# Kernel tuning notes

Hardware: AMD Instinct MI355X
Metric: run time of the kernel (lower is better)

## Reference

```python
import jax, jax.numpy as jnp
import numpy as np

DILATIONS = (1, 2, 4, 8, 16, 32, 64, 128)  # new_dilation doubles across all blocks*layers
BN_EPS = 1e-5


def conv1x1(x, w, b):
    # x: [B,C,N,T], w: [O,C], b: [O]
    return jnp.einsum('oc,bcnt->bont', w, x) + b[None, :, None, None]


def dilated_conv(x, w, b, d):
    T = x.shape[-1]
    y = jnp.einsum('oc,bcnt->bont', w[:, :, 0], x[..., :T - d]) \
      + jnp.einsum('oc,bcnt->bont', w[:, :, 1], x[..., d:])
    return y + b[None, :, None, None]


def graph_conv(x, supports, w, b):
    # gcn module, order=2, diag_mode='self_and_neighbor' (A unchanged), use_power=False
    outs = [x]
    for A in supports:
        h = x
        for _ in range(2):  # order
            h = jnp.einsum('bcvt,vw->bcwt', h, A)  # nconv: 'ncvl,vw->ncwl'
            outs.append(h)
    return conv1x1(jnp.concatenate(outs, axis=1), w, b)


def setup_inputs() -> dict:
    key = jax.random.key(0)
    B, Cin, N, T = 8, 2, 500, 256
    rc, dc, sc, ec, od, L, R = 32, 32, 256, 512, 12, 8, 10
    ks = jax.random.split(key, 24)
    s = 0.1
    return {
        'x': jax.random.normal(ks[0], (B, Cin, N, T), jnp.float32),
        'A0': jax.random.uniform(ks[1], (N, N), jnp.float32),
        'start_w': jax.random.normal(ks[2], (rc, Cin), jnp.float32) * s,
        'start_b': jnp.zeros((rc,), jnp.float32),
        'filt_w': jax.random.normal(ks[3], (L, dc, rc, 2), jnp.float32) * s,
        'filt_b': jnp.zeros((L, dc), jnp.float32),
        'gate_w': jax.random.normal(ks[4], (L, dc, rc, 2), jnp.float32) * s,
        'gate_b': jnp.zeros((L, dc), jnp.float32),
        'skip_w': jax.random.normal(ks[5], (L, sc, dc), jnp.float32) * s,
        'skip_b': jnp.zeros((L, sc), jnp.float32),
        'gcn_w': jax.random.normal(ks[6], (L, rc, 5 * dc), jnp.float32) * s,  # (order*supports+1)*c_in = 160
        'gcn_b': jnp.zeros((L, rc), jnp.float32),
        'bn_g': jnp.ones((L, rc), jnp.float32),
        'bn_b': jnp.zeros((L, rc), jnp.float32),
        'nodevec1': jax.random.normal(ks[7], (N, R), jnp.float32),
        'nodevec2': jax.random.normal(ks[8], (R, N), jnp.float32),
        'end1_w': jax.random.normal(ks[9], (ec, sc), jnp.float32) * s,
        'end1_b': jnp.zeros((ec,), jnp.float32),
        'end2_w': jax.random.normal(ks[10], (od, ec), jnp.float32) * s,
        'end2_b': jnp.zeros((od,), jnp.float32),
    }


def reference(x, A0, start_w, start_b, filt_w, filt_b, gate_w, gate_b,
              skip_w, skip_b, gcn_w, gcn_b, bn_g, bn_b,
              nodevec1, nodevec2, end1_w, end1_b, end2_w, end2_b):
    # adaptive adjacency: softmax(relu(E1 @ E2), dim=1)
    adp = jax.nn.softmax(jax.nn.relu(nodevec1 @ nodevec2), axis=1)
    supports = [A0, adp]

    h = conv1x1(x, start_w, start_b)  # [B,32,N,T]
    skip = None
    for i, d in enumerate(DILATIONS):
        residual = h
        f = jnp.tanh(dilated_conv(residual, filt_w[i], filt_b[i], d))
        g = jax.nn.sigmoid(dilated_conv(residual, gate_w[i], gate_b[i], d))
        h = f * g
        s = conv1x1(h, skip_w[i], skip_b[i])
        skip = s if skip is None else s + skip[..., -s.shape[-1]:]
        h = graph_conv(h, supports, gcn_w[i], gcn_b[i])
        h = h + residual[..., -h.shape[-1]:]
        # BatchNorm2d in eval mode: running_mean=0, running_var=1
        h = h / jnp.sqrt(1.0 + BN_EPS) * bn_g[i][None, :, None, None] + bn_b[i][None, :, None, None]

    out = jax.nn.relu(skip)
    out = jax.nn.relu(conv1x1(out, end1_w, end1_b))
    out = conv1x1(out, end2_w, end2_b)  # [B,12,N,1]
    return out
```

## Files before the change

kernel.cpp:

```cpp
#include <hip/hip_runtime.h>
#include <cstdint>
#include <cstddef>

#define NN 500
#define KP 512

typedef _Float16 f16;
typedef _Float16 half8 __attribute__((ext_vector_type(8)));
typedef float floatx4 __attribute__((ext_vector_type(4)));

struct PassSet {
  const f16* A[10];
  const f16* B[10];
};

__global__ __launch_bounds__(256) void adp_kernel(const float* __restrict__ e1,
                                                  const float* __restrict__ e2,
                                                  float* __restrict__ adp) {
  int r = blockIdx.x;
  int tid = threadIdx.x;
  __shared__ float red[256];
  __shared__ float e1row[16];
  if (tid < 10) e1row[tid] = e1[r * 10 + tid];
  __syncthreads();
  float z0, z1 = 0.f;
  {
    float acc = 0.f;
#pragma unroll
    for (int k = 0; k < 10; k++) acc += e1row[k] * e2[k * NN + tid];
    z0 = fmaxf(acc, 0.f);
  }
  bool has1 = (tid + 256) < NN;
  if (has1) {
    float acc = 0.f;
#pragma unroll
    for (int k = 0; k < 10; k++) acc += e1row[k] * e2[k * NN + tid + 256];
    z1 = fmaxf(acc, 0.f);
  }
  float mx = has1 ? fmaxf(z0, z1) : z0;
  red[tid] = mx;
  __syncthreads();
  for (int s = 128; s > 0; s >>= 1) {
    if (tid < s) red[tid] = fmaxf(red[tid], red[tid + s]);
    __syncthreads();
  }
  mx = red[0];
  __syncthreads();
  float ex0 = __expf(z0 - mx);
  float ex1 = has1 ? __expf(z1 - mx) : 0.f;
  red[tid] = ex0 + ex1;
  __syncthreads();
  for (int s = 128; s > 0; s >>= 1) {
    if (tid < s) red[tid] += red[tid + s];
    __syncthreads();
  }
  float inv = 1.f / red[0];
  adp[r * NN + tid] = ex0 * inv;
  if (has1) adp[r * NN + tid + 256] = ex1 * inv;
}

__global__ __launch_bounds__(256) void xt_kernel(const float* __restrict__ x,
                                                 float* __restrict__ xT) {
  __shared__ float tile[32][33];
  int tx = threadIdx.x & 31, ty = threadIdx.x >> 5;
  int n0 = blockIdx.x * 32, t0 = blockIdx.y * 32, bc = blockIdx.z;
#pragma unroll
  for (int rr = 0; rr < 4; rr++) {
    int n = n0 + ty + rr * 8, t = t0 + tx;
    tile[ty + rr * 8][tx] = (n < NN) ? x[((size_t)bc * NN + n) * 256 + t] : 0.f;
  }
  __syncthreads();
#pragma unroll
  for (int rr = 0; rr < 4; rr++) {
    int t = t0 + ty + rr * 8, n = n0 + tx;
    if (n < NN) xT[((size_t)bc * 256 + t) * NN + n] = tile[tx][ty + rr * 8];
  }
}

__global__ __launch_bounds__(256) void wtr_kernel(const float* __restrict__ fw,
                                                  const float* __restrict__ gw,
                                                  float* __restrict__ fwT,
                                                  float* __restrict__ gwT) {
  int idx = blockIdx.x * 256 + threadIdx.x;
  if (idx >= 16384) return;
  int c = idx & 31;
  int rest = idx >> 5;
  int tap = rest & 1;
  int cpi = rest >> 1;
  int cp = cpi & 31, i = cpi >> 5;
  size_t src = (((size_t)(i * 32 + c) * 32 + cp) * 2) + tap;
  fwT[idx] = fw[src];
  gwT[idx] = gw[src];
}

__global__ __launch_bounds__(256) void bt_kernel(const float* __restrict__ src,
                                                 f16* __restrict__ hi,
                                                 f16* __restrict__ lo) {
  int idx = blockIdx.x * 256 + threadIdx.x;
  int w = idx >> 9, v = idx & 511;
  float x = (w < NN && v < NN) ? src[v * NN + w] : 0.f;
  f16 h = (f16)x;
  hi[idx] = h;
  lo[idx] = (f16)(x - (float)h);
}

__global__ __launch_bounds__(512) void sq_kernel(const float* __restrict__ srcA,
                                                 const float* __restrict__ srcB,
                                                 f16* __restrict__ hiA, f16* __restrict__ loA,
                                                 f16* __restrict__ hiB, f16* __restrict__ loB) {
  const float* src = blockIdx.y == 0 ? srcA : srcB;
  f16* hi = blockIdx.y == 0 ? hiA : hiB;
  f16* lo = blockIdx.y == 0 ? loA : loB;
  int v = blockIdx.x;
  int w = threadIdx.x;
  __shared__ float vrow[512];
  vrow[w] = (v < NN && w < NN) ? src[v * NN + w] : 0.f;
  __syncthreads();
  float acc = 0.f;
  if (v < NN && w < NN) {
#pragma unroll 4
    for (int u = 0; u < NN; u++) acc = fmaf(vrow[u], src[u * NN + w], acc);
  }
  size_t o = (size_t)w * 512 + v;
  f16 h = (f16)acc;
  hi[o] = h;
  lo[o] = (f16)(acc - (float)h);
}

__global__ __launch_bounds__(256) void padzero_kernel(uint32_t* __restrict__ slab, int R) {
  int idx = blockIdx.x * 256 + threadIdx.x;
  int total = 6 * R * 6;
  if (idx >= total) return;
  int a = idx / (R * 6);
  int rem = idx - a * R * 6;
  int row = rem / 6;
  int q = rem - row * 6;
  slab[(size_t)a * R * 256 + (size_t)row * 256 + 250 + q] = 0u;
}

template <bool FUSED>
__global__ __launch_bounds__(256, 4) void dcm_kernel(
    const float* __restrict__ hprev, const float* __restrict__ xT,
    const float* __restrict__ sw, const float* __restrict__ sb,
    const float* __restrict__ fw, const float* __restrict__ fb,
    const float* __restrict__ gw, const float* __restrict__ gb,
    const float* __restrict__ cw, const float* __restrict__ cb,
    float* __restrict__ Hout,
    f16* __restrict__ P1a,
    f16* __restrict__ P2aH, f16* __restrict__ P2aL,
    f16* __restrict__ P1b,
    f16* __restrict__ P2bH, f16* __restrict__ P2bL,
    float* __restrict__ tapL,
    int Lp, int L, int b0) {
  int j = blockIdx.x, bb = blockIdx.y;
  int n0 = blockIdx.z * 256 + threadIdx.x;
  bool ok = (n0 < NN);
  int nc = ok ? n0 : (NN - 1);
  size_t base = ((size_t)(bb * 32) * Lp + 2 * j) * NN;
  size_t cs = (size_t)Lp * NN;
  float x00 = 0.f, x01 = 0.f, x10 = 0.f, x11 = 0.f;
  if (FUSED) {
    const float* xb = xT + (size_t)(b0 + bb) * 2 * 256 * NN;
    x00 = xb[(size_t)(2 * j) * NN + nc];
    x01 = xb[(size_t)(2 * j + 1) * NN + nc];
    x10 = xb[(size_t)(256 + 2 * j) * NN + nc];
    x11 = xb[(size_t)(256 + 2 * j + 1) * NN + nc];
  }
  float accf[32], accg[32];
#pragma unroll
  for (int c = 0; c < 32; c++) {
    accf[c] = fb[c];
    accg[c] = gb[c];
  }
#pragma unroll 2
  for (int cp = 0; cp < 32; cp++) {
    float v0, v1;
    if (FUSED) {
      float w0 = sw[cp * 2], w1 = sw[cp * 2 + 1], bc = sb[cp];
      v0 = fmaf(w0, x00, fmaf(w1, x10, bc));
      v1 = fmaf(w0, x01, fmaf(w1, x11, bc));
    } else {
      const float* hp = hprev + base + cp * cs;
      v0 = hp[nc];
      v1 = hp[NN + nc];
    }
    const float* fwp = fw + cp * 64;
    const float* gwp = gw + cp * 64;
#pragma unroll
    for (int c = 0; c < 32; c++) {
      float fw0 = fwp[c], fw1 = fwp[32 + c];
      float gw0 = gwp[c], gw1 = gwp[32 + c];
      accf[c] = fmaf(fw0, v0, accf[c]);
      accf[c] = fmaf(fw1, v1, accf[c]);
      accg[c] = fmaf(gw0, v0, accg[c]);
      accg[c] = fmaf(gw1, v1, accg[c]);
    }
  }
  float FG[32];
#pragma unroll
  for (int c = 0; c < 32; c++) {
    float E0 = __expf(2.f * accf[c]);
    float th0 = 1.f - 2.f / (E0 + 1.f);
    float sg0 = 1.f / (1.f + __expf(-accg[c]));
    FG[c] = th0 * sg0;
  }
  if (j == L - 1 && ok) {
    size_t tbase = ((size_t)(b0 + bb) * 32) * NN;
#pragma unroll
    for (int c = 0; c < 32; c++) {
      tapL[tbase + (size_t)c * NN + n0] = FG[c];
    }
  }
  if (Hout == nullptr) return;
#pragma unroll 2
  for (int c = 0; c < 32; c++) {
    const float* wr = cw + c * 160;
    float cbc = cb[c];
    float h0 = cbc, p10 = 0.f, p20 = 0.f, q10 = 0.f, q20 = 0.f;
#pragma unroll
    for (int cp = 0; cp < 32; cp++) {
      float w0 = wr[cp], w1 = wr[32 + cp], w2 = wr[64 + cp];
      float w3 = wr[96 + cp], w4 = wr[128 + cp];
      float f0 = FG[cp];
      h0  = fmaf(w0, f0, h0);
      p10 = fmaf(w1, f0, p10);
      p20 = fmaf(w2, f0, p20);
      q10 = fmaf(w3, f0, q10);
      q20 = fmaf(w4, f0, q20);
    }
    if (FUSED) {
      float sw0 = sw[c * 2], sw1 = sw[c * 2 + 1], sbc = sb[c];
      h0 += fmaf(sw0, x01, fmaf(sw1, x11, sbc));
    } else {
      const float* hr = hprev + ((size_t)(bb * 32 + c) * Lp + 2 * j + 1) * NN;
      h0 += hr[nc];
    }
    if (ok) {
      size_t mi = (size_t)(bb * 32 + c) * L + j;
      size_t o = mi * KP;
      f16 t;
      Hout[mi * NN + n0] = h0;
      P1a[o + n0] = (f16)p10;
      t = (f16)p20; P2aH[o + n0] = t; P2aL[o + n0] = (f16)(p20 - (float)t);
      P1b[o + n0] = (f16)q10;
      t = (f16)q20; P2bH[o + n0] = t; P2bL[o + n0] = (f16)(q20 - (float)t);
    }
  }
}

__global__ __launch_bounds__(256) void mfma_gcn(PassSet s,
    const float* __restrict__ Cin, float* __restrict__ Out, int M,
    const float* __restrict__ bng, const float* __restrict__ bnb, int lshift) {
  __shared__ f16 As[128 * 32];
  __shared__ f16 Bs[128 * 32];
  int tid = threadIdx.x;
  int wave = tid >> 6, lane = tid & 63;
  int wm = wave >> 1, wn = wave & 1;
  int m0 = blockIdx.x * 128;
  int n0 = blockIdx.y * 128;
  int lm = lane & 15, kq = lane >> 4;
  int srow = tid >> 2, sc = tid & 3;
  int ar0 = m0 + srow;      if (ar0 > M - 1) ar0 = M - 1;
  int ar1 = m0 + srow + 64; if (ar1 > M - 1) ar1 = M - 1;
  size_t ag0 = (size_t)ar0 * KP + sc * 8;
  size_t ag1 = (size_t)ar1 * KP + sc * 8;
  size_t bg0 = (size_t)(n0 + srow) * KP + sc * 8;
  size_t bg1 = (size_t)(n0 + srow + 64) * KP + sc * 8;
  int sl0 = srow * 32 + ((sc ^ ((srow >> 1) & 3)) << 3);
  int sl1 = sl0 + 64 * 32;
  int ach = kq ^ ((lm >> 1) & 3);

  floatx4 acc[4][4];
#pragma unroll
  for (int i = 0; i < 4; i++)
#pragma unroll
    for (int j = 0; j < 4; j++) acc[i][j] = (floatx4){0.f, 0.f, 0.f, 0.f};

  float4 pa0, pa1, pb0, pb1;
  {
    const f16* Ap = s.A[0];
    const f16* Bp = s.B[0];
    pa0 = *(const float4*)(Ap + ag0);
    pa1 = *(const float4*)(Ap + ag1);
    pb0 = *(const float4*)(Bp + bg0);
    pb1 = *(const float4*)(Bp + bg1);
  }
#pragma unroll
  for (int p = 0; p < 10; p++) {
    const f16* __restrict__ Ap = s.A[p];
    const f16* __restrict__ Bp = s.B[p];
    const f16* __restrict__ Apn = s.A[p < 9 ? p + 1 : p];
    const f16* __restrict__ Bpn = s.B[p < 9 ? p + 1 : p];
    for (int k0 = 0; k0 < KP; k0 += 32) {
      __syncthreads();
      *(float4*)(As + sl0) = pa0;
      *(float4*)(As + sl1) = pa1;
      *(float4*)(Bs + sl0) = pb0;
      *(float4*)(Bs + sl1) = pb1;
      __syncthreads();
      {
        bool lastk = (k0 == KP - 32);
        const f16* An = lastk ? Apn : Ap;
        const f16* Bn = lastk ? Bpn : Bp;
        int kn = lastk ? 0 : k0 + 32;
        pa0 = *(const float4*)(An + ag0 + kn);
        pa1 = *(const float4*)(An + ag1 + kn);
        pb0 = *(const float4*)(Bn + bg0 + kn);
        pb1 = *(const float4*)(Bn + bg1 + kn);
      }
      half8 a[4];
#pragma unroll
      for (int i = 0; i < 4; i++)
        a[i] = *(const half8*)(As + (wm * 64 + i * 16 + lm) * 32 + ach * 8);
#pragma unroll
      for (int j = 0; j < 4; j++) {
        half8 b = *(const half8*)(Bs + (wn * 64 + j * 16 + lm) * 32 + ach * 8);
#pragma unroll
        for (int i = 0; i < 4; i++)
          acc[i][j] = __builtin_amdgcn_mfma_f32_16x16x32_f16(a[i], b, acc[i][j], 0, 0, 0);
      }
    }
  }
  int cn = lane & 15, rq = lane >> 4;
  float rs = rsqrtf(1.f + 1e-5f);
#pragma unroll
  for (int i = 0; i < 4; i++) {
#pragma unroll
    for (int r = 0; r < 4; r++) {
      int row = m0 + wm * 64 + i * 16 + rq * 4 + r;
      if (row < M) {
        int c = (row >> lshift) & 31;
        float scale = bng[c] * rs;
        float bias = bnb[c];
#pragma unroll
        for (int j = 0; j < 4; j++) {
          int col = n0 + wn * 64 + j * 16 + cn;
          if (col < NN) {
            size_t o = (size_t)row * NN + col;
            Out[o] = (acc[i][j][r] + Cin[o]) * scale + bias;
          }
        }
      }
    }
  }
}

#define NB 20
#define NBP 21
__global__ __launch_bounds__(256) void final_kernel(const float* __restrict__ tap,
    const float* __restrict__ skw, const float* __restrict__ skb,
    const float* __restrict__ e1w, const float* __restrict__ e1b,
    const float* __restrict__ e2w, const float* __restrict__ e2b,
    float* __restrict__ out) {
  __shared__ float tapS[256][NBP];
  __shared__ float skS[256][NBP];
  __shared__ float e1S[512][NBP];
  int tid = threadIdx.x;
  int b = blockIdx.y;
  int n0 = blockIdx.x * NB;
  {
    int i = tid >> 5, c = tid & 31;
    const float* tp = tap + (((size_t)i * 8 + b) * 32 + c) * NN + n0;
#pragma unroll
    for (int v = 0; v < NB; v++) tapS[tid][v] = tp[v];
  }
  __syncthreads();
  {
    float bsum = 0.f;
#pragma unroll
    for (int i2 = 0; i2 < 8; i2++) bsum += skb[i2 * 256 + tid];
    float acc[NB];
#pragma unroll
    for (int v = 0; v < NB; v++) acc[v] = bsum;
#pragma unroll
    for (int i2 = 0; i2 < 8; i2++) {
      const float* wr = skw + ((size_t)i2 * 256 + tid) * 32;
#pragma unroll
      for (int cp = 0; cp < 32; cp++) {
        float w = wr[cp];
#pragma unroll
        for (int v = 0; v < NB; v++) acc[v] = fmaf(w, tapS[i2 * 32 + cp][v], acc[v]);
      }
    }
#pragma unroll
    for (int v = 0; v < NB; v++) skS[tid][v] = fmaxf(acc[v], 0.f);
  }
  __syncthreads();
#pragma unroll
  for (int h = 0; h < 2; h++) {
    int k = tid + h * 256;
    float bv = e1b[k];
    float acc[NB];
#pragma unroll
    for (int v = 0; v < NB; v++) acc[v] = bv;
    const float* wr = e1w + (size_t)k * 256;
    for (int o = 0; o < 256; o++) {
      float w = wr[o];
#pragma unroll
      for (int v = 0; v < NB; v++) acc[v] = fmaf(w, skS[o][v], acc[v]);
    }
#pragma unroll
    for (int v = 0; v < NB; v++) e1S[k][v] = fmaxf(acc[v], 0.f);
  }
  __syncthreads();
  if (tid < 12 * NB) {
    int q = tid / NB, v = tid % NB;
    float acc = e2b[q];
    const float* wr = e2w + (size_t)q * 512;
#pragma unroll 8
    for (int k = 0; k < 512; k++) acc = fmaf(wr[k], e1S[k][v], acc);
    out[((size_t)b * 12 + q) * NN + n0 + v] = acc;
  }
}

extern "C" void kernel_launch(void* const* d_in, const int* in_sizes, int n_in,
                              void* d_out, int out_size, void* d_ws, size_t ws_size,
                              hipStream_t stream) {
  const float* x       = (const float*)d_in[0];
  const float* A0      = (const float*)d_in[1];
  const float* start_w = (const float*)d_in[2];
  const float* start_b = (const float*)d_in[3];
  const float* filt_w  = (const float*)d_in[4];
  const float* filt_b  = (const float*)d_in[5];
  const float* gate_w  = (const float*)d_in[6];
  const float* gate_b  = (const float*)d_in[7];
  const float* skip_w  = (const float*)d_in[8];
  const float* skip_b  = (const float*)d_in[9];
  const float* gcn_w   = (const float*)d_in[10];
  const float* gcn_b   = (const float*)d_in[11];
  const float* bn_g    = (const float*)d_in[12];
  const float* bn_b    = (const float*)d_in[13];
  const float* nv1     = (const float*)d_in[14];
  const float* nv2     = (const float*)d_in[15];
  const float* e1w     = (const float*)d_in[16];
  const float* e1b     = (const float*)d_in[17];
  const float* e2w     = (const float*)d_in[18];
  const float* e2b     = (const float*)d_in[19];
  float* out = (float*)d_out;

  char* ws = (char*)d_ws;
  size_t off = 0;
  auto alloc = [&](size_t bytes) -> void* {
    void* p = (void*)(ws + off);
    off += (bytes + 255) & ~(size_t)255;
    return p;
  };
  float* adp   = (float*)alloc((size_t)NN * NN * 4);
  float* tap   = (float*)alloc((size_t)8 * 8 * 32 * NN * 4);
  float* xT    = (float*)alloc((size_t)16 * 256 * NN * 4);
  float* fwT   = (float*)alloc((size_t)16384 * 4);
  float* gwT   = (float*)alloc((size_t)16384 * 4);
  f16*   A0tH  = (f16*)alloc((size_t)KP * KP * 2);
  f16*   A0tL  = (f16*)alloc((size_t)KP * KP * 2);
  f16*   adptH = (f16*)alloc((size_t)KP * KP * 2);
  f16*   adptL = (f16*)alloc((size_t)KP * KP * 2);
  f16*   Q0H   = (f16*)alloc((size_t)KP * KP * 2);
  f16*   Q0L   = (f16*)alloc((size_t)KP * KP * 2);
  f16*   QdH   = (f16*)alloc((size_t)KP * KP * 2);
  f16*   QdL   = (f16*)alloc((size_t)KP * KP * 2);
  size_t fixed = off;

  int g = 1, rpb = 512;
  {
    const int gcand[4] = {8, 4, 2, 1};
    const int rcand[4] = {4096, 2048, 1024, 512};
    bool found = false;
    for (int gi = 0; gi < 4 && !found; gi++) {
      for (int ri = 0; ri < 4 && !found; ri++) {
        int gg = gcand[gi], rr = rcand[ri];
        if (4096 / rr > gg) continue;
        size_t need = fixed + (size_t)gg * 12288000ull +
                      6ull * gg * rr * KP * 2 + (1u << 20);
        if (need <= ws_size) { g = gg; rpb = rr; found = true; }
      }
    }
  }
  float* h128 = (float*)alloc((size_t)g * 8192000ull);
  float* h64  = (float*)alloc((size_t)g * 4096000ull);
  int R = g * rpb;
  f16* slab   = (f16*)alloc(6ull * R * KP * 2);
  f16* P1a  = slab + 0ull * R * KP;
  f16* P2aH = slab + 1ull * R * KP;
  f16* P2aL = slab + 2ull * R * KP;
  f16* P1b  = slab + 3ull * R * KP;
  f16* P2bH = slab + 4ull * R * KP;
  f16* P2bL = slab + 5ull * R * KP;

  adp_kernel<<<NN, 256, 0, stream>>>(nv1, nv2, adp);
  xt_kernel<<<dim3(16, 8, 16), 256, 0, stream>>>(x, xT);
  wtr_kernel<<<64, 256, 0, stream>>>(filt_w, gate_w, fwT, gwT);
  bt_kernel<<<1024, 256, 0, stream>>>(A0, A0tH, A0tL);
  bt_kernel<<<1024, 256, 0, stream>>>(adp, adptH, adptL);
  sq_kernel<<<dim3(512, 2), 512, 0, stream>>>(A0, adp, Q0H, Q0L, QdH, QdL);
  padzero_kernel<<<(36 * R + 255) / 256, 256, 0, stream>>>((uint32_t*)slab, R);

  PassSet ps{};
  {
    const f16* Alist[10] = {P1a, P1a, P2aH, P2aH, P2aL, P1b, P1b, P2bH, P2bH, P2bL};
    const f16* Blist[10] = {A0tH, A0tL, Q0H, Q0L, Q0H, adptH, adptL, QdH, QdL, QdH};
    for (int q = 0; q < 10; q++) { ps.A[q] = Alist[q]; ps.B[q] = Blist[q]; }
  }

  for (int b0 = 0; b0 < 8; b0 += g) {
    float* hprev = nullptr;
    int Lp = 256;
    for (int i = 0; i < 8; i++) {
      int L = Lp >> 1;
      if (i < 7) {
        float* hout = (i & 1) ? h64 : h128;
        int rows = 32 * L;
        int nCh = (rows + rpb - 1) / rpb;
        if (nCh < 1) nCh = 1;
        int bbw = g / nCh;
        for (int ch = 0; ch < nCh; ch++) {
          int bb0 = ch * bbw;
          const float* hprev_c = hprev ? hprev + (size_t)bb0 * 32 * Lp * NN : nullptr;
          float* hout_c = hout + (size_t)bb0 * 32 * L * NN;
          if (i == 0) {
            dcm_kernel<true><<<dim3(L, bbw, 2), 256, 0, stream>>>(
                nullptr, xT, start_w, start_b,
                fwT + i * 2048, filt_b + i * 32, gwT + i * 2048, gate_b + i * 32,
                gcn_w + i * 5120, gcn_b + i * 32, hout_c,
                P1a, P2aH, P2aL, P1b, P2bH, P2bL,
                tap + (size_t)i * 8 * 32 * NN, Lp, L, b0 + bb0);
          } else {
            dcm_kernel<false><<<dim3(L, bbw, 2), 256, 0, stream>>>(
                hprev_c, nullptr, nullptr, nullptr,
                fwT + i * 2048, filt_b + i * 32, gwT + i * 2048, gate_b + i * 32,
                gcn_w + i * 5120, gcn_b + i * 32, hout_c,
                P1a, P2aH, P2aL, P1b, P2bH, P2bL,
                tap + (size_t)i * 8 * 32 * NN, Lp, L, b0 + bb0);
          }
          int M = bbw * 32 * L;
          int Mb = (M + 127) / 128;
          mfma_gcn<<<dim3(Mb, 4), 256, 0, stream>>>(ps, hout_c, hout_c, M,
                                                    bn_g + i * 32, bn_b + i * 32, 7 - i);
        }
        hprev = hout;
        Lp = L;
      } else {
        dcm_kernel<false><<<dim3(1, g, 2), 256, 0, stream>>>(
            hprev, nullptr, nullptr, nullptr,
            fwT + i * 2048, filt_b + i * 32, gwT + i * 2048, gate_b + i * 32,
            gcn_w, gcn_b, nullptr,
            P1a, P2aH, P2aL, P1b, P2bH, P2bL,
            tap + (size_t)i * 8 * 32 * NN, Lp, 1, b0);
      }
    }
  }
  final_kernel<<<dim3(25, 8), 256, 0, stream>>>(tap, skip_w, skip_b, e1w, e1b, e2w, e2b, out);
}
```

Baseline: 2.052 ms.

## Double-buffer GCN GEMM tiles using direct global-to-LDS async loads

The MFMA graph-conv GEMM no longer stages tiles through registers with two barriers per k-step. It now issues global_load_lds 16-byte loads straight into a second LDS buffer while the current buffer is consumed, using a partial vmcnt wait and a single barrier before compute. This targets register pressure and the exposed load latency between k-steps. The earlier clamp of A rows to M-1 is gone, so the last M-tile may read past the valid rows unless the buffers are padded. The manual waitcnt and sched barriers also tie correctness to the exact load count per thread.

```diff
diff --git a/kernel.cpp b/kernel.cpp
--- a/kernel.cpp
+++ b/kernel.cpp
@@ -8,6 +8,11 @@
 typedef _Float16 f16;
 typedef _Float16 half8 __attribute__((ext_vector_type(8)));
 typedef float floatx4 __attribute__((ext_vector_type(4)));
+
+#define GLOAD16(gp, lp)                                                     \
+  __builtin_amdgcn_global_load_lds(                                         \
+      (const __attribute__((address_space(1))) void*)(gp),                  \
+      (__attribute__((address_space(3))) void*)(lp), 16, 0, 0)
 
 struct PassSet {
   const f16* A[10];
@@ -251,23 +256,19 @@
 __global__ __launch_bounds__(256) void mfma_gcn(PassSet s,
     const float* __restrict__ Cin, float* __restrict__ Out, int M,
     const float* __restrict__ bng, const float* __restrict__ bnb, int lshift) {
-  __shared__ f16 As[128 * 32];
-  __shared__ f16 Bs[128 * 32];
+  __shared__ f16 As[2][128 * 32];
+  __shared__ f16 Bs[2][128 * 32];
   int tid = threadIdx.x;
   int wave = tid >> 6, lane = tid & 63;
   int wm = wave >> 1, wn = wave & 1;
   int m0 = blockIdx.x * 128;
   int n0 = blockIdx.y * 128;
   int lm = lane & 15, kq = lane >> 4;
-  int srow = tid >> 2, sc = tid & 3;
-  int ar0 = m0 + srow;      if (ar0 > M - 1) ar0 = M - 1;
-  int ar1 = m0 + srow + 64; if (ar1 > M - 1) ar1 = M - 1;
-  size_t ag0 = (size_t)ar0 * KP + sc * 8;
-  size_t ag1 = (size_t)ar1 * KP + sc * 8;
-  size_t bg0 = (size_t)(n0 + srow) * KP + sc * 8;
-  size_t bg1 = (size_t)(n0 + srow + 64) * KP + sc * 8;
-  int sl0 = srow * 32 + ((sc ^ ((srow >> 1) & 3)) << 3);
-  int sl1 = sl0 + 64 * 32;
+  int laneoff = (lane >> 2) * KP + (((lane & 3) ^ ((lane >> 3) & 3)) << 3);
+  int r0 = 32 * wave;
+  size_t agA = (size_t)(m0 + r0) * KP + laneoff;
+  size_t agB = (size_t)(n0 + r0) * KP + laneoff;
+  int l0 = r0 * 32 + (lane << 3);
   int ach = kq ^ ((lm >> 1) & 3);
 
   floatx4 acc[4][4];
@@ -276,15 +277,16 @@
 #pragma unroll
     for (int j = 0; j < 4; j++) acc[i][j] = (floatx4){0.f, 0.f, 0.f, 0.f};
 
-  float4 pa0, pa1, pb0, pb1;
   {
     const f16* Ap = s.A[0];
     const f16* Bp = s.B[0];
-    pa0 = *(const float4*)(Ap + ag0);
-    pa1 = *(const float4*)(Ap + ag1);
-    pb0 = *(const float4*)(Bp + bg0);
-    pb1 = *(const float4*)(Bp + bg1);
-  }
+#pragma unroll
+    for (int q = 0; q < 2; q++) {
+      GLOAD16(Ap + agA + q * 16 * KP, &As[0][l0 + q * 512]);
+      GLOAD16(Bp + agB + q * 16 * KP, &Bs[0][l0 + q * 512]);
+    }
+  }
+  int cur = 0;
 #pragma unroll
   for (int p = 0; p < 10; p++) {
     const f16* __restrict__ Ap = s.A[p];
@@ -292,35 +294,43 @@
     const f16* __restrict__ Apn = s.A[p < 9 ? p + 1 : p];
     const f16* __restrict__ Bpn = s.B[p < 9 ? p + 1 : p];
     for (int k0 = 0; k0 < KP; k0 += 32) {
-      __syncthreads();
-      *(float4*)(As + sl0) = pa0;
-      *(float4*)(As + sl1) = pa1;
-      *(float4*)(Bs + sl0) = pb0;
-      *(float4*)(Bs + sl1) = pb1;
-      __syncthreads();
       {
         bool lastk = (k0 == KP - 32);
         const f16* An = lastk ? Apn : Ap;
         const f16* Bn = lastk ? Bpn : Bp;
         int kn = lastk ? 0 : k0 + 32;
-        pa0 = *(const float4*)(An + ag0 + kn);
-        pa1 = *(const float4*)(An + ag1 + kn);
-        pb0 = *(const float4*)(Bn + bg0 + kn);
-        pb1 = *(const float4*)(Bn + bg1 + kn);
+        f16* Adst = &As[cur ^ 1][l0];
+        f16* Bdst = &Bs[cur ^ 1][l0];
+#pragma unroll
+        for (int q = 0; q < 2; q++) {
+          GLOAD16(An + agA + q * 16 * KP + kn, Adst + q * 512);
+          GLOAD16(Bn + agB + q * 16 * KP + kn, Bdst + q * 512);
+        }
       }
+      __builtin_amdgcn_sched_barrier(0);
+      asm volatile("s_waitcnt vmcnt(4)" ::: "memory");
+      __builtin_amdgcn_s_barrier();
+      __builtin_amdgcn_sched_barrier(0);
+      const f16* Ac = As[cur];
+      const f16* Bc = Bs[cur];
       half8 a[4];
 #pragma unroll
       for (int i = 0; i < 4; i++)
-        a[i] = *(const half8*)(As + (wm * 64 + i * 16 + lm) * 32 + ach * 8);
+        a[i] = *(const half8*)(Ac + (wm * 64 + i * 16 + lm) * 32 + ach * 8);
 #pragma unroll
       for (int j = 0; j < 4; j++) {
-        half8 b = *(const half8*)(Bs + (wn * 64 + j * 16 + lm) * 32 + ach * 8);
+        half8 b = *(const half8*)(Bc + (wn * 64 + j * 16 + lm) * 32 + ach * 8);
 #pragma unroll
         for (int i = 0; i < 4; i++)
           acc[i][j] = __builtin_amdgcn_mfma_f32_16x16x32_f16(a[i], b, acc[i][j], 0, 0, 0);
       }
-    }
-  }
+      __builtin_amdgcn_sched_barrier(0);
+      __builtin_amdgcn_s_barrier();
+      __builtin_amdgcn_sched_barrier(0);
+      cur ^= 1;
+    }
+  }
+  asm volatile("s_waitcnt vmcnt(0)" ::: "memory");
   int cn = lane & 15, rq = lane >> 4;
   float rs = rsqrtf(1.f + 1e-5f);
 #pragma unroll
```

Result: no change. 2.070 ms (+0.8%).
